# Optimization experiments

Measured on AMD Instinct MI355X. Metric: run time of the kernel, lower is better.

## Reference

```python
import jax, jax.numpy as jnp
import numpy as np

NHEAD = 16      # config['transformer_nheads']
N_LAYERS = 2    # config['layers']
EPS = 1e-5      # torch LayerNorm default


def _layernorm(x, w, b):
    m = jnp.mean(x, axis=-1, keepdims=True)
    v = jnp.var(x, axis=-1, keepdims=True)
    return (x - m) * jax.lax.rsqrt(v + EPS) * w + b


def _mha_causal(h, wqkv, bqkv, wo, bo):
    # Causal self-attention == running the encoder on every growing prefix and
    # keeping the last position (the original O(T^2) python loop), since the
    # encoder layer has no positional encoding and all other ops are per-token.
    B, T, H = h.shape
    hd = H // NHEAD
    qkv = h @ wqkv.T + bqkv                       # [B,T,3H]
    q, k, v = jnp.split(qkv, 3, axis=-1)
    q = q.reshape(B, T, NHEAD, hd)
    k = k.reshape(B, T, NHEAD, hd)
    v = v.reshape(B, T, NHEAD, hd)
    scale = jnp.asarray(1.0 / np.sqrt(hd), h.dtype)
    scores = jnp.einsum('bqhd,bkhd->bhqk', q, k) * scale
    mask = jnp.tril(jnp.ones((T, T), dtype=bool))  # query q attends to keys <= q
    scores = jnp.where(mask, scores, jnp.asarray(-1e9, h.dtype))
    attn = jax.nn.softmax(scores, axis=-1)
    out = jnp.einsum('bhqk,bkhd->bqhd', attn, v).reshape(B, T, H)
    return out @ wo.T + bo


def _encoder_layer(h, in_proj_w, in_proj_b, out_proj_w, out_proj_b,
                   ln1_w, ln1_b, ff1_w, ff1_b, ff2_w, ff2_b, ln2_w, ln2_b):
    # PyTorch TransformerEncoderLayer, post-norm, relu, eval mode (no dropout)
    a = _mha_causal(h, in_proj_w, in_proj_b, out_proj_w, out_proj_b)
    h = _layernorm(h + a, ln1_w, ln1_b)
    f = jax.nn.relu(h @ ff1_w.T + ff1_b) @ ff2_w.T + ff2_b
    return _layernorm(h + f, ln2_w, ln2_b)


def _lstm(xs, h0, c0, w_ih, w_hh, b_ih, b_hh):
    # PyTorch single-layer LSTM, gate order (i, f, g, o)
    def step(carry, x_t):
        h, c = carry
        g = x_t @ w_ih.T + b_ih + h @ w_hh.T + b_hh
        i, f, gg, o = jnp.split(g, 4, axis=-1)
        c = jax.nn.sigmoid(f) * c + jax.nn.sigmoid(i) * jnp.tanh(gg)
        h = jax.nn.sigmoid(o) * jnp.tanh(c)
        return (h, c), h
    (hT, cT), ys = jax.lax.scan(step, (h0, c0), jnp.swapaxes(xs, 0, 1))
    return jnp.swapaxes(ys, 0, 1), hT, cT


def _forward(x, user_vector, game_vector, fc_w, fc_b,
             in_proj_w, in_proj_b, out_proj_w, out_proj_b,
             ln1_w, ln1_b, ff1_w, ff1_b, ff2_w, ff2_b, ln2_w, ln2_b,
             lstm_w_ih, lstm_w_hh, lstm_b_ih, lstm_b_hh,
             out1_w, out1_b, out2_w, out2_b):
    h = jax.nn.relu(x @ fc_w.T + fc_b)            # fc (dropout off in eval)
    uv, gv = user_vector, game_vector
    lstm_out = h
    for j in range(N_LAYERS):
        enc = _encoder_layer(h, in_proj_w, in_proj_b, out_proj_w, out_proj_b,
                             ln1_w, ln1_b, ff1_w, ff1_b, ff2_w, ff2_b, ln2_w, ln2_b)
        lstm_out, hT, cT = _lstm(enc, uv[:, j, :], gv[:, j, :],
                                 lstm_w_ih, lstm_w_hh, lstm_b_ih, lstm_b_hh)
        h = lstm_out
        uv = uv.at[:, j, :].set(hT)
        gv = gv.at[:, j, :].set(cT)
    o = jax.nn.relu(lstm_out @ out1_w.T + out1_b) @ out2_w.T + out2_b
    return jax.nn.log_softmax(o, axis=-1), gv, uv


def setup_inputs() -> dict:
    B, T, D, H, FF, OUT = 256, 10, 512, 1024, 2048, 2
    L = N_LAYERS
    key = jax.random.key(0)
    ks = jax.random.split(key, 20)
    def w(k, shape, fan_in):
        return (jax.random.normal(k, shape, jnp.float32) / np.sqrt(fan_in)).astype(jnp.float32)
    z = lambda shape: jnp.zeros(shape, jnp.float32)
    return {
        'x': jax.random.normal(ks[0], (B, T, D), jnp.float32),
        'user_vector': jax.random.normal(ks[1], (B, L, H), jnp.float32),
        'game_vector': jax.random.normal(ks[2], (B, L, H), jnp.float32),
        'fc_w': w(ks[3], (H, D), D), 'fc_b': z((H,)),
        'in_proj_w': w(ks[4], (3 * H, H), H), 'in_proj_b': z((3 * H,)),
        'out_proj_w': w(ks[5], (H, H), H), 'out_proj_b': z((H,)),
        'ln1_w': jnp.ones((H,), jnp.float32), 'ln1_b': z((H,)),
        'ff1_w': w(ks[6], (FF, H), H), 'ff1_b': z((FF,)),
        'ff2_w': w(ks[7], (H, FF), FF), 'ff2_b': z((H,)),
        'ln2_w': jnp.ones((H,), jnp.float32), 'ln2_b': z((H,)),
        'lstm_w_ih': w(ks[8], (4 * H, H), H), 'lstm_w_hh': w(ks[9], (4 * H, H), H),
        'lstm_b_ih': z((4 * H,)), 'lstm_b_hh': z((4 * H,)),
        'out1_w': w(ks[10], (H // 2, H), H), 'out1_b': z((H // 2,)),
        'out2_w': w(ks[11], (OUT, H // 2), H // 2), 'out2_b': z((OUT,)),
    }


def reference(x, user_vector, game_vector, fc_w, fc_b,
              in_proj_w, in_proj_b, out_proj_w, out_proj_b,
              ln1_w, ln1_b, ff1_w, ff1_b, ff2_w, ff2_b, ln2_w, ln2_b,
              lstm_w_ih, lstm_w_hh, lstm_b_ih, lstm_b_hh,
              out1_w, out1_b, out2_w, out2_b):
    return _forward(x, user_vector, game_vector, fc_w, fc_b,
                    in_proj_w, in_proj_b, out_proj_w, out_proj_b,
                    ln1_w, ln1_b, ff1_w, ff1_b, ff2_w, ff2_b, ln2_w, ln2_b,
                    lstm_w_ih, lstm_w_hh, lstm_b_ih, lstm_b_hh,
                    out1_w, out1_b, out2_w, out2_b)
```

## Files before the change

kernel.cpp:

```cpp
#include <hip/hip_runtime.h>
#include <math.h>

#define B_    256
#define T_    10
#define D_    512
#define H_    1024
#define FF_   2048
#define NHEAD 16
#define HD    64
#define M_    (B_ * T_)
#define NL    2

typedef unsigned short u16;
typedef unsigned int   u32;
typedef __attribute__((ext_vector_type(8))) short bf16x8;
typedef __attribute__((ext_vector_type(4))) float f32x4;

__device__ inline float sigmoidf_(float x) { return 1.0f / (1.0f + expf(-x)); }
__device__ inline float b2f(u16 v) { return __uint_as_float(((u32)v) << 16); }
__device__ inline u16 f2b(float f) {
    u32 u = __float_as_uint(f);
    return (u16)((u + 0x7fffu + ((u >> 16) & 1u)) >> 16);
}

struct u16x8 { u16 v[8]; };

__global__ __launch_bounds__(256) void cvt_weights(
    const float* __restrict__ fcw, const float* __restrict__ inp,
    const float* __restrict__ outp, const float* __restrict__ f1,
    const float* __restrict__ f2, const float* __restrict__ wih,
    const float* __restrict__ whh, const float* __restrict__ o1w,
    const float* __restrict__ xin,
    u16* __restrict__ wb)
{
    const int e = (blockIdx.x * 256 + threadIdx.x) * 8;
    const float* src; int off;
    if      (e <   524288) { src = fcw;  off = 0; }
    else if (e <  3670016) { src = inp;  off = 524288; }
    else if (e <  4718592) { src = outp; off = 3670016; }
    else if (e <  6815744) { src = f1;   off = 4718592; }
    else if (e <  8912896) { src = f2;   off = 6815744; }
    else if (e < 13107200) { src = wih;  off = 8912896; }
    else if (e < 17301504) { src = whh;  off = 13107200; }
    else if (e < 17825792) { src = o1w;  off = 17301504; }
    else                   { src = xin;  off = 17825792; }
    const float* p = src + (e - off);
    const float4 x0 = *((const float4*)p);
    const float4 x1 = *((const float4*)(p + 4));
    u16x8 r;
    r.v[0] = f2b(x0.x); r.v[1] = f2b(x0.y); r.v[2] = f2b(x0.z); r.v[3] = f2b(x0.w);
    r.v[4] = f2b(x1.x); r.v[5] = f2b(x1.y); r.v[6] = f2b(x1.z); r.v[7] = f2b(x1.w);
    *((u16x8*)(wb + e)) = r;
}

template<int BM, int BN, bool RELU, bool WF32, bool WB16>
__global__ __launch_bounds__(256) void gemm_mfma(const u16* __restrict__ A,
                                                 const u16* __restrict__ W,
                                                 const float* __restrict__ bias,
                                                 float* __restrict__ Cf,
                                                 u16* __restrict__ Cb,
                                                 int M, int N, int K)
{
    constexpr int MI = BM / 32;
    constexpr int NJ = BN / 32;
    __shared__ alignas(16) u16 As[2 * BM * 32];
    __shared__ alignas(16) u16 Bs[2 * BN * 32];

    int bx, by;
    {
        const int gx = gridDim.x, gy = gridDim.y;
        const int total = gx * gy;
        const int id = blockIdx.y * gx + blockIdx.x;
        if (((total & 7) == 0) && ((gy & 3) == 0)) {
            const int per = total >> 3;
            const int lid = (id & 7) * per + (id >> 3);
            const int band = gx << 2;
            const int g = lid / band;
            const int r = lid - g * band;
            by = (g << 2) + (r & 3);
            bx = r >> 2;
        } else { bx = blockIdx.x; by = blockIdx.y; }
    }

    const int wave = threadIdx.x >> 6;
    const int lane = threadIdx.x & 63;
    const int m0 = by * BM;
    const int n0 = bx * BN;
    const int wm = (wave >> 1) * (BM / 2);
    const int wn = (wave & 1) * (BN / 2);
    const int lr = lane >> 2;
    const int lc = (lane & 3) * 8;
    const int fr = lane & 15;
    const int kq = lane >> 4;

    f32x4 acc[MI][NJ] = {};

    for (int k0 = 0; k0 < K; k0 += 64) {
#pragma unroll
        for (int cc = 0; cc < BM / 64; ++cc) {
            const int c = cc * 4 + wave;
            const u16* g = A + (size_t)(m0 + c * 16 + lr) * K + k0 + lc;
#pragma unroll
            for (int kk = 0; kk < 2; ++kk)
                __builtin_amdgcn_global_load_lds(
                    (const __attribute__((address_space(1))) void*)(g + kk * 32),
                    (__attribute__((address_space(3))) void*)(As + kk * BM * 32 + c * 512), 16, 0, 0);
        }
#pragma unroll
        for (int cc = 0; cc < BN / 64; ++cc) {
            const int c = cc * 4 + wave;
            const u16* g = W + (size_t)(n0 + c * 16 + lr) * K + k0 + lc;
#pragma unroll
            for (int kk = 0; kk < 2; ++kk)
                __builtin_amdgcn_global_load_lds(
                    (const __attribute__((address_space(1))) void*)(g + kk * 32),
                    (__attribute__((address_space(3))) void*)(Bs + kk * BN * 32 + c * 512), 16, 0, 0);
        }
        __syncthreads();

#pragma unroll
        for (int kk = 0; kk < 2; ++kk) {
            bf16x8 a[MI], b[NJ];
#pragma unroll
            for (int i = 0; i < MI; ++i)
                a[i] = *(const bf16x8*)(As + kk * BM * 32 + (wm + i * 16 + fr) * 32 + kq * 8);
#pragma unroll
            for (int j = 0; j < NJ; ++j)
                b[j] = *(const bf16x8*)(Bs + kk * BN * 32 + (wn + j * 16 + fr) * 32 + kq * 8);
#pragma unroll
            for (int i = 0; i < MI; ++i)
#pragma unroll
                for (int j = 0; j < NJ; ++j)
                    acc[i][j] = __builtin_amdgcn_mfma_f32_16x16x32_bf16(a[i], b[j], acc[i][j], 0, 0, 0);
        }
        __syncthreads();
    }

#pragma unroll
    for (int i = 0; i < MI; ++i) {
#pragma unroll
        for (int j = 0; j < NJ; ++j) {
            const int col = n0 + wn + j * 16 + fr;
            const float bv = bias ? bias[col] : 0.0f;
#pragma unroll
            for (int r = 0; r < 4; ++r) {
                const int row = m0 + wm + i * 16 + kq * 4 + r;
                float v = acc[i][j][r] + bv;
                if (RELU) v = fmaxf(v, 0.0f);
                if (WF32) Cf[(size_t)row * N + col] = v;
                if (WB16) Cb[(size_t)row * N + col] = f2b(v);
            }
        }
    }
}

__global__ __launch_bounds__(256) void lstm_step(const u16* __restrict__ h_in,
                                                 const u16* __restrict__ Whh,
                                                 const u16* __restrict__ gx,
                                                 float* __restrict__ cstate,
                                                 u16* __restrict__ h_out,
                                                 float* __restrict__ lout_f,
                                                 u16* __restrict__ lout_b,
                                                 int t,
                                                 float* __restrict__ hT_out,
                                                 float* __restrict__ cT_out)
{
    __shared__ alignas(16) u16 Bs[4 * 64 * 32];
    __shared__ alignas(16) char region[64 * 65 * 4];
    u16*  As  = (u16*)region;
    float* ghs = (float*)region;

    const int j0 = blockIdx.x * 16;
    const int b0 = blockIdx.y * 64;

    const int wave = threadIdx.x >> 6;
    const int lane = threadIdx.x & 63;
    const int wm = (wave >> 1) * 32;
    const int wn = (wave & 1) * 32;
    const int lr = lane >> 2;
    const int lc = (lane & 3) * 8;
    const int fr = lane & 15;
    const int kq = lane >> 4;

    f32x4 acc[2][2] = {};

    for (int k0 = 0; k0 < H_; k0 += 128) {
        {
            const u16* g = h_in + (size_t)(b0 + wave * 16 + lr) * H_ + k0 + lc;
#pragma unroll
            for (int kk = 0; kk < 4; ++kk)
                __builtin_amdgcn_global_load_lds(
                    (const __attribute__((address_space(1))) void*)(g + kk * 32),
                    (__attribute__((address_space(3))) void*)(As + kk * 2048 + wave * 512), 16, 0, 0);
        }
        {
            const u16* g = Whh + (size_t)(wave * H_ + j0 + lr) * H_ + k0 + lc;
#pragma unroll
            for (int kk = 0; kk < 4; ++kk)
                __builtin_amdgcn_global_load_lds(
                    (const __attribute__((address_space(1))) void*)(g + kk * 32),
                    (__attribute__((address_space(3))) void*)(Bs + kk * 2048 + wave * 512), 16, 0, 0);
        }
        __syncthreads();

#pragma unroll
        for (int kk = 0; kk < 4; ++kk) {
            bf16x8 a[2], b[2];
#pragma unroll
            for (int i = 0; i < 2; ++i)
                a[i] = *(const bf16x8*)(As + kk * 2048 + (wm + i * 16 + fr) * 32 + kq * 8);
#pragma unroll
            for (int j = 0; j < 2; ++j)
                b[j] = *(const bf16x8*)(Bs + kk * 2048 + (wn + j * 16 + fr) * 32 + kq * 8);
#pragma unroll
            for (int i = 0; i < 2; ++i)
#pragma unroll
                for (int j = 0; j < 2; ++j)
                    acc[i][j] = __builtin_amdgcn_mfma_f32_16x16x32_bf16(a[i], b[j], acc[i][j], 0, 0, 0);
        }
        __syncthreads();
    }

#pragma unroll
    for (int i = 0; i < 2; ++i)
#pragma unroll
        for (int j = 0; j < 2; ++j) {
            const int rl = wn + j * 16 + fr;
#pragma unroll
            for (int r = 0; r < 4; ++r) {
                const int bl = wm + i * 16 + kq * 4 + r;
                ghs[bl * 65 + rl] = acc[i][j][r];
            }
        }
    __syncthreads();

    {
        const int bl = threadIdx.x >> 2;
        const int jq = threadIdx.x & 3;
        const int b_ = b0 + bl;
        const int jbase = jq * 4;
        const u16* g1 = gx + (size_t)(b_ * T_ + t) * (4 * H_) + j0 + jbase;
        float hh4[4], c4[4];
#pragma unroll
        for (int q = 0; q < 4; ++q) {
            const int jj = jbase + q;
            const float gi = b2f(g1[q])          + ghs[bl * 65 +  0 + jj];
            const float gf = b2f(g1[H_ + q])     + ghs[bl * 65 + 16 + jj];
            const float gg = b2f(g1[2 * H_ + q]) + ghs[bl * 65 + 32 + jj];
            const float go = b2f(g1[3 * H_ + q]) + ghs[bl * 65 + 48 + jj];
            const int sid = b_ * H_ + j0 + jbase + q;
            const float c  = sigmoidf_(gf) * cstate[sid] + sigmoidf_(gi) * tanhf(gg);
            const float hh = sigmoidf_(go) * tanhf(c);
            cstate[sid] = c;
            c4[q] = c;
            hh4[q] = hh;
        }
        u16*   hp = h_out  + (size_t)b_ * H_ + j0 + jbase;
        float* lf = lout_f + (size_t)(b_ * T_ + t) * H_ + j0 + jbase;
        u16*   lb = lout_b + (size_t)(b_ * T_ + t) * H_ + j0 + jbase;
#pragma unroll
        for (int q = 0; q < 4; ++q) {
            const u16 hb16 = f2b(hh4[q]);
            hp[q] = hb16;
            lf[q] = hh4[q];
            lb[q] = hb16;
        }
        if (hT_out) {
#pragma unroll
            for (int q = 0; q < 4; ++q) {
                hT_out[(size_t)b_ * (NL * H_) + j0 + jbase + q] = hh4[q];
                cT_out[(size_t)b_ * (NL * H_) + j0 + jbase + q] = c4[q];
            }
        }
    }
}

__global__ __launch_bounds__(256) void attn_kernel(const u16* __restrict__ qkv,
                                                   u16* __restrict__ ctx)
{
    const int bh = blockIdx.x;
    const int b  = bh >> 4;
    const int h  = bh & 15;

    __shared__ float q[T_][HD], k[T_][HD], v[T_][HD];
    __shared__ float p[T_][T_];

    for (int idx = threadIdx.x; idx < T_ * HD; idx += 256) {
        const int t = idx >> 6, d = idx & 63;
        const u16* row = qkv + (size_t)(b * T_ + t) * (3 * H_) + h * HD + d;
        q[t][d] = b2f(row[0]);
        k[t][d] = b2f(row[H_]);
        v[t][d] = b2f(row[2 * H_]);
    }
    __syncthreads();

    if (threadIdx.x < T_ * T_) {
        const int qi = threadIdx.x / T_, ki = threadIdx.x % T_;
        float s = 0.0f;
        if (ki <= qi) {
            for (int d = 0; d < HD; ++d) s = fmaf(q[qi][d], k[ki][d], s);
            s *= 0.125f;
        }
        p[qi][ki] = s;
    }
    __syncthreads();

    if (threadIdx.x < T_) {
        const int rq = threadIdx.x;
        float mx = -1e30f;
        for (int ki = 0; ki <= rq; ++ki) mx = fmaxf(mx, p[rq][ki]);
        float sum = 0.0f;
        for (int ki = 0; ki <= rq; ++ki) { const float e = expf(p[rq][ki] - mx); p[rq][ki] = e; sum += e; }
        const float inv = 1.0f / sum;
        for (int ki = 0; ki <= rq; ++ki) p[rq][ki] *= inv;
        for (int ki = rq + 1; ki < T_; ++ki) p[rq][ki] = 0.0f;
    }
    __syncthreads();

    for (int idx = threadIdx.x; idx < T_ * HD; idx += 256) {
        const int t = idx >> 6, d = idx & 63;
        float s = 0.0f;
        for (int ki = 0; ki <= t; ++ki) s = fmaf(p[t][ki], v[ki][d], s);
        ctx[(size_t)(b * T_ + t) * H_ + h * HD + d] = f2b(s);
    }
}

__global__ __launch_bounds__(256) void ln_kernel(const float* __restrict__ x,
                                                 const float* __restrict__ res,
                                                 const float* __restrict__ w,
                                                 const float* __restrict__ b,
                                                 float* __restrict__ outf,
                                                 u16* __restrict__ outb)
{
    const int row = blockIdx.x;
    const float* xr = x + (size_t)row * H_;
    const float* rr = res + (size_t)row * H_;

    float vals[4];
    float s = 0.0f, s2 = 0.0f;
#pragma unroll
    for (int i = 0; i < 4; ++i) {
        const int c = threadIdx.x + i * 256;
        const float vv = xr[c] + rr[c];
        vals[i] = vv;
        s += vv;
        s2 = fmaf(vv, vv, s2);
    }
    for (int off = 32; off; off >>= 1) {
        s  += __shfl_down(s, off);
        s2 += __shfl_down(s2, off);
    }
    __shared__ float rs_[4], rs2_[4];
    const int wave = threadIdx.x >> 6, lane = threadIdx.x & 63;
    if (lane == 0) { rs_[wave] = s; rs2_[wave] = s2; }
    __syncthreads();
    const float st  = rs_[0] + rs_[1] + rs_[2] + rs_[3];
    const float st2 = rs2_[0] + rs2_[1] + rs2_[2] + rs2_[3];
    const float m   = st * (1.0f / 1024.0f);
    const float var = st2 * (1.0f / 1024.0f) - m * m;
    const float rsv = rsqrtf(var + 1e-5f);
#pragma unroll
    for (int i = 0; i < 4; ++i) {
        const int c = threadIdx.x + i * 256;
        const float v = (vals[i] - m) * rsv * w[c] + b[c];
        if (outf) outf[(size_t)row * H_ + c] = v;
        if (outb) outb[(size_t)row * H_ + c] = f2b(v);
    }
}

__global__ __launch_bounds__(256) void init_states(const float* __restrict__ uvec,
                                                   const float* __restrict__ gvec,
                                                   int layer,
                                                   u16* __restrict__ hstate_b,
                                                   float* __restrict__ cstate)
{
    const int id = blockIdx.x * 256 + threadIdx.x;
    const int b  = id >> 10;
    const int j  = id & 1023;
    hstate_b[id] = f2b(uvec[(size_t)(b * NL + layer) * H_ + j]);
    cstate[id]   = gvec[(size_t)(b * NL + layer) * H_ + j];
}

__global__ __launch_bounds__(256) void bias_sum(const float* __restrict__ a,
                                                const float* __restrict__ b,
                                                float* __restrict__ o)
{
    const int i = blockIdx.x * 256 + threadIdx.x;
    o[i] = a[i] + b[i];
}

__global__ __launch_bounds__(256) void head_kernel(const float* __restrict__ o1,
                                                   const float* __restrict__ w2,
                                                   const float* __restrict__ b2,
                                                   float* __restrict__ out)
{
    const int token = blockIdx.x * 4 + (threadIdx.x >> 6);
    const int lane  = threadIdx.x & 63;
    const float* row = o1 + (size_t)token * (H_ / 2);
    float s0 = 0.0f, s1 = 0.0f;
    for (int c = lane; c < H_ / 2; c += 64) {
        const float xv = row[c];
        s0 = fmaf(xv, w2[c], s0);
        s1 = fmaf(xv, w2[H_ / 2 + c], s1);
    }
    for (int off = 32; off; off >>= 1) {
        s0 += __shfl_down(s0, off);
        s1 += __shfl_down(s1, off);
    }
    if (lane == 0) {
        const float o0 = s0 + b2[0];
        const float o1v = s1 + b2[1];
        const float mx = fmaxf(o0, o1v);
        const float lse = mx + logf(expf(o0 - mx) + expf(o1v - mx));
        out[(size_t)token * 2 + 0] = o0 - lse;
        out[(size_t)token * 2 + 1] = o1v - lse;
    }
}

extern "C" void kernel_launch(void* const* d_in, const int* in_sizes, int n_in,
                              void* d_out, int out_size, void* d_ws, size_t ws_size,
                              hipStream_t stream)
{
    const float* x         = (const float*)d_in[0];
    const float* user_vec  = (const float*)d_in[1];
    const float* game_vec  = (const float*)d_in[2];
    const float* fc_w      = (const float*)d_in[3];
    const float* fc_b      = (const float*)d_in[4];
    const float* in_proj_w = (const float*)d_in[5];
    const float* in_proj_b = (const float*)d_in[6];
    const float* out_proj_w= (const float*)d_in[7];
    const float* out_proj_b= (const float*)d_in[8];
    const float* ln1_w     = (const float*)d_in[9];
    const float* ln1_b     = (const float*)d_in[10];
    const float* ff1_w     = (const float*)d_in[11];
    const float* ff1_b     = (const float*)d_in[12];
    const float* ff2_w     = (const float*)d_in[13];
    const float* ff2_b     = (const float*)d_in[14];
    const float* ln2_w     = (const float*)d_in[15];
    const float* ln2_b     = (const float*)d_in[16];
    const float* w_ih      = (const float*)d_in[17];
    const float* w_hh      = (const float*)d_in[18];
    const float* b_ih      = (const float*)d_in[19];
    const float* b_hh      = (const float*)d_in[20];
    const float* out1_w    = (const float*)d_in[21];
    const float* out1_b    = (const float*)d_in[22];
    const float* out2_w    = (const float*)d_in[23];
    const float* out2_b    = (const float*)d_in[24];
    float* out = (float*)d_out;

    char* base = (char*)d_ws;
    u16* wb = (u16*)base;
    u16* fc_wb   = wb;
    u16* inp_wb  = wb + 524288;
    u16* outp_wb = wb + 3670016;
    u16* ff1_wb  = wb + 4718592;
    u16* ff2_wb  = wb + 6815744;
    u16* wih_b   = wb + 8912896;
    u16* whh_b   = wb + 13107200;
    u16* out1_wb = wb + 17301504;
    u16* x_b     = wb + 17825792;
    char* A1 = base + 38273024;
    char* S1 = A1 + 20971520;
    char* S2 = S1 + 10485760;
    u16*  hb = (u16*)(S2 + 5242880);
    float* buf0 = (float*)((char*)hb + 5242880);
    float* cstate = (float*)((char*)buf0 + 10485760);
    u16*  hs0 = (u16*)((char*)cstate + 1048576);
    u16*  hs1 = (u16*)((char*)hs0 + 524288);
    float* bsum = (float*)((char*)hs1 + 524288);

    u16*   qkv_b = (u16*)A1;
    float* tmp1  = (float*)A1;
    float* tmp2  = (float*)(A1 + 10485760);
    u16*   gx_b  = (u16*)A1;
    float* o1    = (float*)A1;
    u16*   ff1b  = (u16*)S1;
    u16*   ctx_b = (u16*)S2;
    u16*   ln1b  = (u16*)S2;
    u16*   enc_b = (u16*)S2;

    float* gv_out = out + (size_t)M_ * 2;
    float* uv_out = gv_out + (size_t)B_ * NL * H_;

    hipLaunchKernelGGL(bias_sum, dim3(4 * H_ / 256), dim3(256), 0, stream, b_ih, b_hh, bsum);
    hipLaunchKernelGGL(cvt_weights, dim3(19136512 / 8 / 256), dim3(256), 0, stream,
                       fc_w, in_proj_w, out_proj_w, ff1_w, ff2_w, w_ih, w_hh, out1_w,
                       x, wb);

    hipLaunchKernelGGL((gemm_mfma<64, 128, true, true, true>),
                       dim3(H_ / 128, M_ / 64), dim3(256), 0, stream,
                       x_b, fc_wb, fc_b, buf0, hb, M_, H_, D_);

    for (int layer = 0; layer < NL; ++layer) {
        hipLaunchKernelGGL((gemm_mfma<128, 128, false, false, true>),
                           dim3(3 * H_ / 128, M_ / 128), dim3(256), 0, stream,
                           hb, inp_wb, in_proj_b, (float*)nullptr, qkv_b, M_, 3 * H_, H_);
        hipLaunchKernelGGL(attn_kernel, dim3(B_ * NHEAD), dim3(256), 0, stream, qkv_b, ctx_b);
        hipLaunchKernelGGL((gemm_mfma<64, 128, false, true, false>),
                           dim3(H_ / 128, M_ / 64), dim3(256), 0, stream,
                           ctx_b, outp_wb, out_proj_b, tmp1, (u16*)nullptr, M_, H_, H_);
        hipLaunchKernelGGL(ln_kernel, dim3(M_), dim3(256), 0, stream,
                           buf0, tmp1, ln1_w, ln1_b, tmp2, ln1b);
        hipLaunchKernelGGL((gemm_mfma<128, 128, true, false, true>),
                           dim3(FF_ / 128, M_ / 128), dim3(256), 0, stream,
                           ln1b, ff1_wb, ff1_b, (float*)nullptr, ff1b, M_, FF_, H_);
        hipLaunchKernelGGL((gemm_mfma<64, 128, false, true, false>),
                           dim3(H_ / 128, M_ / 64), dim3(256), 0, stream,
                           ff1b, ff2_wb, ff2_b, tmp1, (u16*)nullptr, M_, H_, FF_);
        hipLaunchKernelGGL(ln_kernel, dim3(M_), dim3(256), 0, stream,
                           tmp2, tmp1, ln2_w, ln2_b, (float*)nullptr, enc_b);
        hipLaunchKernelGGL((gemm_mfma<128, 128, false, false, true>),
                           dim3(4 * H_ / 128, M_ / 128), dim3(256), 0, stream,
                           enc_b, wih_b, bsum, (float*)nullptr, gx_b, M_, 4 * H_, H_);
        hipLaunchKernelGGL(init_states, dim3(B_ * H_ / 256), dim3(256), 0, stream,
                           user_vec, game_vec, layer, hs0, cstate);
        for (int t = 0; t < T_; ++t) {
            const bool last = (t == T_ - 1);
            hipLaunchKernelGGL(lstm_step, dim3(64, 4), dim3(256), 0, stream,
                               (t & 1) ? hs1 : hs0, whh_b, gx_b, cstate,
                               (t & 1) ? hs0 : hs1, buf0, hb, t,
                               last ? (uv_out + layer * H_) : nullptr,
                               last ? (gv_out + layer * H_) : nullptr);
        }
    }

    hipLaunchKernelGGL((gemm_mfma<64, 64, true, true, false>),
                       dim3((H_ / 2) / 64, M_ / 64), dim3(256), 0, stream,
                       hb, out1_wb, out1_b, o1, (u16*)nullptr, M_, H_ / 2, H_);
    hipLaunchKernelGGL(head_kernel, dim3(M_ / 4), dim3(256), 0, stream, o1, out2_w, out2_b, out);
}
```

Before: 789.5 us.

## Double-buffer LDS tiles in GEMM and LSTM step kernels; fold LSTM biases

```diff
diff --git a/kernel.cpp b/kernel.cpp
--- a/kernel.cpp
+++ b/kernel.cpp
@@ -63,8 +63,10 @@
 {
     constexpr int MI = BM / 32;
     constexpr int NJ = BN / 32;
-    __shared__ alignas(16) u16 As[2 * BM * 32];
-    __shared__ alignas(16) u16 Bs[2 * BN * 32];
+    constexpr int ASZ = 2 * BM * 32;
+    constexpr int BSZ = 2 * BN * 32;
+    __shared__ alignas(16) u16 As[2 * ASZ];
+    __shared__ alignas(16) u16 Bs[2 * BSZ];
 
     int bx, by;
     {
@@ -93,9 +95,7 @@
     const int fr = lane & 15;
     const int kq = lane >> 4;
 
-    f32x4 acc[MI][NJ] = {};
-
-    for (int k0 = 0; k0 < K; k0 += 64) {
+    auto stage = [&](int buf, int k0) {
 #pragma unroll
         for (int cc = 0; cc < BM / 64; ++cc) {
             const int c = cc * 4 + wave;
@@ -104,7 +104,7 @@
             for (int kk = 0; kk < 2; ++kk)
                 __builtin_amdgcn_global_load_lds(
                     (const __attribute__((address_space(1))) void*)(g + kk * 32),
-                    (__attribute__((address_space(3))) void*)(As + kk * BM * 32 + c * 512), 16, 0, 0);
+                    (__attribute__((address_space(3))) void*)(As + buf * ASZ + kk * BM * 32 + c * 512), 16, 0, 0);
         }
 #pragma unroll
         for (int cc = 0; cc < BN / 64; ++cc) {
@@ -114,19 +114,26 @@
             for (int kk = 0; kk < 2; ++kk)
                 __builtin_amdgcn_global_load_lds(
                     (const __attribute__((address_space(1))) void*)(g + kk * 32),
-                    (__attribute__((address_space(3))) void*)(Bs + kk * BN * 32 + c * 512), 16, 0, 0);
-        }
-        __syncthreads();
-
+                    (__attribute__((address_space(3))) void*)(Bs + buf * BSZ + kk * BN * 32 + c * 512), 16, 0, 0);
+        }
+    };
+
+    f32x4 acc[MI][NJ] = {};
+
+    stage(0, 0);
+    __syncthreads();
+    int cur = 0;
+    for (int k0 = 0; k0 < K; k0 += 64) {
+        if (k0 + 64 < K) stage(cur ^ 1, k0 + 64);
 #pragma unroll
         for (int kk = 0; kk < 2; ++kk) {
             bf16x8 a[MI], b[NJ];
 #pragma unroll
             for (int i = 0; i < MI; ++i)
-                a[i] = *(const bf16x8*)(As + kk * BM * 32 + (wm + i * 16 + fr) * 32 + kq * 8);
+                a[i] = *(const bf16x8*)(As + cur * ASZ + kk * BM * 32 + (wm + i * 16 + fr) * 32 + kq * 8);
 #pragma unroll
             for (int j = 0; j < NJ; ++j)
-                b[j] = *(const bf16x8*)(Bs + kk * BN * 32 + (wn + j * 16 + fr) * 32 + kq * 8);
+                b[j] = *(const bf16x8*)(Bs + cur * BSZ + kk * BN * 32 + (wn + j * 16 + fr) * 32 + kq * 8);
 #pragma unroll
             for (int i = 0; i < MI; ++i)
 #pragma unroll
@@ -134,6 +141,7 @@
                     acc[i][j] = __builtin_amdgcn_mfma_f32_16x16x32_bf16(a[i], b[j], acc[i][j], 0, 0, 0);
         }
         __syncthreads();
+        cur ^= 1;
     }
 
 #pragma unroll
@@ -157,6 +165,8 @@
 __global__ __launch_bounds__(256) void lstm_step(const u16* __restrict__ h_in,
                                                  const u16* __restrict__ Whh,
                                                  const u16* __restrict__ gx,
+                                                 const float* __restrict__ bih,
+                                                 const float* __restrict__ bhh,
                                                  float* __restrict__ cstate,
                                                  u16* __restrict__ h_out,
                                                  float* __restrict__ lout_f,
@@ -165,10 +175,8 @@
                                                  float* __restrict__ hT_out,
                                                  float* __restrict__ cT_out)
 {
-    __shared__ alignas(16) u16 Bs[4 * 64 * 32];
-    __shared__ alignas(16) char region[64 * 65 * 4];
-    u16*  As  = (u16*)region;
-    float* ghs = (float*)region;
+    __shared__ alignas(16) u16 smem[2 * 16384];
+    float* ghs = (float*)smem;
 
     const int j0 = blockIdx.x * 16;
     const int b0 = blockIdx.y * 64;
@@ -182,27 +190,30 @@
     const int fr = lane & 15;
     const int kq = lane >> 4;
 
+    auto stage = [&](int buf, int k0) {
+        const u16* ga = h_in + (size_t)(b0 + wave * 16 + lr) * H_ + k0 + lc;
+#pragma unroll
+        for (int kk = 0; kk < 4; ++kk)
+            __builtin_amdgcn_global_load_lds(
+                (const __attribute__((address_space(1))) void*)(ga + kk * 32),
+                (__attribute__((address_space(3))) void*)(smem + buf * 16384 + kk * 2048 + wave * 512), 16, 0, 0);
+        const u16* gb = Whh + (size_t)(wave * H_ + j0 + lr) * H_ + k0 + lc;
+#pragma unroll
+        for (int kk = 0; kk < 4; ++kk)
+            __builtin_amdgcn_global_load_lds(
+                (const __attribute__((address_space(1))) void*)(gb + kk * 32),
+                (__attribute__((address_space(3))) void*)(smem + buf * 16384 + 8192 + kk * 2048 + wave * 512), 16, 0, 0);
+    };
+
     f32x4 acc[2][2] = {};
 
+    stage(0, 0);
+    __syncthreads();
+    int cur = 0;
     for (int k0 = 0; k0 < H_; k0 += 128) {
-        {
-            const u16* g = h_in + (size_t)(b0 + wave * 16 + lr) * H_ + k0 + lc;
-#pragma unroll
-            for (int kk = 0; kk < 4; ++kk)
-                __builtin_amdgcn_global_load_lds(
-                    (const __attribute__((address_space(1))) void*)(g + kk * 32),
-                    (__attribute__((address_space(3))) void*)(As + kk * 2048 + wave * 512), 16, 0, 0);
-        }
-        {
-            const u16* g = Whh + (size_t)(wave * H_ + j0 + lr) * H_ + k0 + lc;
-#pragma unroll
-            for (int kk = 0; kk < 4; ++kk)
-                __builtin_amdgcn_global_load_lds(
-                    (const __attribute__((address_space(1))) void*)(g + kk * 32),
-                    (__attribute__((address_space(3))) void*)(Bs + kk * 2048 + wave * 512), 16, 0, 0);
-        }
-        __syncthreads();
-
+        if (k0 + 128 < H_) stage(cur ^ 1, k0 + 128);
+        const u16* As = smem + cur * 16384;
+        const u16* Bs = As + 8192;
 #pragma unroll
         for (int kk = 0; kk < 4; ++kk) {
             bf16x8 a[2], b[2];
@@ -219,6 +230,7 @@
                     acc[i][j] = __builtin_amdgcn_mfma_f32_16x16x32_bf16(a[i], b[j], acc[i][j], 0, 0, 0);
         }
         __syncthreads();
+        cur ^= 1;
     }
 
 #pragma unroll
@@ -244,11 +256,12 @@
 #pragma unroll
         for (int q = 0; q < 4; ++q) {
             const int jj = jbase + q;
-            const float gi = b2f(g1[q])          + ghs[bl * 65 +  0 + jj];
-            const float gf = b2f(g1[H_ + q])     + ghs[bl * 65 + 16 + jj];
-            const float gg = b2f(g1[2 * H_ + q]) + ghs[bl * 65 + 32 + jj];
-            const float go = b2f(g1[3 * H_ + q]) + ghs[bl * 65 + 48 + jj];
-            const int sid = b_ * H_ + j0 + jbase + q;
+            const int jg = j0 + jbase + q;
+            const float gi = b2f(g1[q])          + bih[jg]           + bhh[jg]           + ghs[bl * 65 +  0 + jj];
+            const float gf = b2f(g1[H_ + q])     + bih[H_ + jg]      + bhh[H_ + jg]      + ghs[bl * 65 + 16 + jj];
+            const float gg = b2f(g1[2 * H_ + q]) + bih[2 * H_ + jg]  + bhh[2 * H_ + jg]  + ghs[bl * 65 + 32 + jj];
+            const float go = b2f(g1[3 * H_ + q]) + bih[3 * H_ + jg]  + bhh[3 * H_ + jg]  + ghs[bl * 65 + 48 + jj];
+            const int sid = b_ * H_ + jg;
             const float c  = sigmoidf_(gf) * cstate[sid] + sigmoidf_(gi) * tanhf(gg);
             const float hh = sigmoidf_(go) * tanhf(c);
             cstate[sid] = c;
@@ -379,14 +392,6 @@
     const int j  = id & 1023;
     hstate_b[id] = f2b(uvec[(size_t)(b * NL + layer) * H_ + j]);
     cstate[id]   = gvec[(size_t)(b * NL + layer) * H_ + j];
-}
-
-__global__ __launch_bounds__(256) void bias_sum(const float* __restrict__ a,
-                                                const float* __restrict__ b,
-                                                float* __restrict__ o)
-{
-    const int i = blockIdx.x * 256 + threadIdx.x;
-    o[i] = a[i] + b[i];
 }
 
 __global__ __launch_bounds__(256) void head_kernel(const float* __restrict__ o1,
@@ -467,7 +472,6 @@
     float* cstate = (float*)((char*)buf0 + 10485760);
     u16*  hs0 = (u16*)((char*)cstate + 1048576);
     u16*  hs1 = (u16*)((char*)hs0 + 524288);
-    float* bsum = (float*)((char*)hs1 + 524288);
 
     u16*   qkv_b = (u16*)A1;
     float* tmp1  = (float*)A1;
@@ -482,7 +486,6 @@
     float* gv_out = out + (size_t)M_ * 2;
     float* uv_out = gv_out + (size_t)B_ * NL * H_;
 
-    hipLaunchKernelGGL(bias_sum, dim3(4 * H_ / 256), dim3(256), 0, stream, b_ih, b_hh, bsum);
     hipLaunchKernelGGL(cvt_weights, dim3(19136512 / 8 / 256), dim3(256), 0, stream,
                        fc_w, in_proj_w, out_proj_w, ff1_w, ff2_w, w_ih, w_hh, out1_w,
                        x, wb);
@@ -511,13 +514,13 @@
                            tmp2, tmp1, ln2_w, ln2_b, (float*)nullptr, enc_b);
         hipLaunchKernelGGL((gemm_mfma<128, 128, false, false, true>),
                            dim3(4 * H_ / 128, M_ / 128), dim3(256), 0, stream,
-                           enc_b, wih_b, bsum, (float*)nullptr, gx_b, M_, 4 * H_, H_);
+                           enc_b, wih_b, (const float*)nullptr, (float*)nullptr, gx_b, M_, 4 * H_, H_);
         hipLaunchKernelGGL(init_states, dim3(B_ * H_ / 256), dim3(256), 0, stream,
                            user_vec, game_vec, layer, hs0, cstate);
         for (int t = 0; t < T_; ++t) {
             const bool last = (t == T_ - 1);
             hipLaunchKernelGGL(lstm_step, dim3(64, 4), dim3(256), 0, stream,
-                               (t & 1) ? hs1 : hs0, whh_b, gx_b, cstate,
+                               (t & 1) ? hs1 : hs0, whh_b, gx_b, b_ih, b_hh, cstate,
                                (t & 1) ? hs0 : hs1, buf0, hb, t,
                                last ? (uv_out + layer * H_) : nullptr,
                                last ? (gv_out + layer * H_) : nullptr);
```

After: 777.8 us. About the same (-1.5%).
